# Kernel optimization log

Hardware: AMD Instinct MI355X
Metric: run time of the kernel (lower is better)

The kernel has to match this reference:

```python
import jax, jax.numpy as jnp
import numpy as np

B, T = 65536, 256
E = H = 5

def setup_inputs() -> dict:
    key = jax.random.key(0)
    ks = jax.random.split(key, 8)
    return {
        "x": jax.random.randint(ks[0], (B, T), 0, 2),
        "emb": jax.random.normal(ks[1], (2, E), jnp.float32),
        "W_ih": jax.random.normal(ks[2], (4 * H, E), jnp.float32) * 0.3,
        "W_hh": jax.random.normal(ks[3], (4 * H, H), jnp.float32) * 0.3,
        "b_ih": jax.random.normal(ks[4], (4 * H,), jnp.float32) * 0.1,
        "b_hh": jax.random.normal(ks[5], (4 * H,), jnp.float32) * 0.1,
        "W_lin": jax.random.normal(ks[6], (2, H), jnp.float32) * 0.3,
        "b_lin": jax.random.normal(ks[7], (2,), jnp.float32) * 0.1,
    }

def reference(x, emb, W_ih, W_hh, b_ih, b_hh, W_lin, b_lin):
    # Embedding lookup: [B, T] int -> [B, T, E]
    xe = emb[x]
    # Precompute input contributions to all 4 gates for every timestep: [B, T, 4H]
    gx = jnp.einsum("bte,ge->btg", xe, W_ih) + (b_ih + b_hh)
    Whh_T = W_hh.T  # [H, 4H]

    def step(carry, gx_t):
        h, c = carry  # each [B, H]
        gates = gx_t + h @ Whh_T  # [B, 4H]
        i, f, g, o = jnp.split(gates, 4, axis=-1)  # PyTorch gate order i,f,g,o
        i = jax.nn.sigmoid(i)
        f = jax.nn.sigmoid(f)
        g = jnp.tanh(g)
        o = jax.nn.sigmoid(o)
        c = f * c + i * g
        h = o * jnp.tanh(c)
        return (h, c), None

    h0 = jnp.zeros((x.shape[0], H), xe.dtype)
    c0 = jnp.zeros((x.shape[0], H), xe.dtype)
    # scan over time (axis 1 -> move to leading axis)
    (h_last, _), _ = jax.lax.scan(step, (h0, c0), jnp.swapaxes(gx, 0, 1))
    # Final-step linear head: [B, H] -> [B, 2]
    return h_last @ W_lin.T + b_lin
```

## Files before the change

kernel.cpp:

```cpp
#include <hip/hip_runtime.h>


typedef float v2f __attribute__((ext_vector_type(2)));

constexpr int TT = 256;

__device__ __forceinline__ float fexp2(float v) { return __builtin_amdgcn_exp2f(v); }
__device__ __forceinline__ float frcp(float v)  { return __builtin_amdgcn_rcpf(v); }

__device__ __forceinline__ int pair_row(int p, int h) {
    if (p < 8) return (p >> 1) * 5 + (p & 1) * 2 + h;
    return (p == 8) ? (h ? 9 : 4) : (h ? 19 : 14);
}

__global__ __launch_bounds__(256, 1) void lstm_fused(
    const int* __restrict__ x,
    const float* __restrict__ emb,
    const float* __restrict__ W_ih,
    const float* __restrict__ W_hh,
    const float* __restrict__ b_ih,
    const float* __restrict__ b_hh,
    const float* __restrict__ W_lin,
    const float* __restrict__ b_lin,
    float* __restrict__ out)
{
    const int b = blockIdx.x * blockDim.x + threadIdx.x;

    const float NL2E  = -1.4426950408889634f;
    const float T2L2E =  2.8853900817779268f;
    const v2f ONE = {1.f, 1.f};
    const v2f T2v = {T2L2E, T2L2E};

    v2f bpk[10], dpk[10];
    v2f wpk[5][10];
#pragma unroll
    for (int p = 0; p < 10; ++p) {
        float v0[2], v1[2];
#pragma unroll
        for (int h = 0; h < 2; ++h) {
            const int r = pair_row(p, h);
            const float s = (r >= 10 && r < 15) ? T2L2E : NL2E;
            float g0 = b_ih[r] + b_hh[r], g1 = g0;
#pragma unroll
            for (int e = 0; e < 5; ++e) {
                float w = W_ih[r * 5 + e];
                g0 = fmaf(w, emb[e],     g0);
                g1 = fmaf(w, emb[5 + e], g1);
            }
            v0[h] = s * g0;
            v1[h] = s * (g1 - g0);
#pragma unroll
            for (int k = 0; k < 5; ++k) {
                float w = s * W_hh[r * 5 + k];
                asm volatile("" : "+v"(w));
                wpk[k][p][h] = w;
            }
        }
        asm volatile("" : "+v"(v0[0]), "+v"(v0[1]), "+v"(v1[0]), "+v"(v1[1]));
        bpk[p][0] = v0[0]; bpk[p][1] = v0[1];
        dpk[p][0] = v1[0]; dpk[p][1] = v1[1];
    }

    v2f chat01 = {0.f, 0.f}, chat23 = {0.f, 0.f};
    float chat4 = 0.f;
    v2f h01 = {0.f, 0.f}, h23 = {0.f, 0.f};
    float h4 = 0.f;

    auto step = [&](int xt) {
        const float xtf = (float)xt;
        v2f xv; xv[0] = xtf; xv[1] = xtf;
        v2f g[10];
#pragma unroll
        for (int p = 0; p < 10; ++p)
            g[p] = __builtin_elementwise_fma(xv, dpk[p], bpk[p]);
        const float hk[5] = {h01[0], h01[1], h23[0], h23[1], h4};
#pragma unroll
        for (int k = 0; k < 5; ++k) {
            v2f hv; hv[0] = hk[k]; hv[1] = hk[k];
#pragma unroll
            for (int p = 0; p < 10; ++p)
                g[p] = __builtin_elementwise_fma(wpk[k][p], hv, g[p]);
        }
        v2f E[10];
#pragma unroll
        for (int p = 0; p < 10; ++p) {
            E[p][0] = fexp2(g[p][0]);
            E[p][1] = fexp2(g[p][1]);
        }

        v2f Ai01 = E[0] + ONE, Af01 = E[2] + ONE, Ag01 = E[4] + ONE;
        v2f P01 = Ai01 * Ag01, D01 = P01 * Af01;
        v2f t01 = __builtin_elementwise_fma(T2v, E[4], -T2v);
        v2f N01 = __builtin_elementwise_fma(chat01, P01, t01 * Af01);

        v2f Ai23 = E[1] + ONE, Af23 = E[3] + ONE, Ag23 = E[5] + ONE;
        v2f P23 = Ai23 * Ag23, D23 = P23 * Af23;
        v2f t23 = __builtin_elementwise_fma(T2v, E[5], -T2v);
        v2f N23 = __builtin_elementwise_fma(chat23, P23, t23 * Af23);

        v2f AiAf4 = E[8] + ONE;
        v2f AgAo4 = E[9] + ONE;
        float P4 = AiAf4[0] * AgAo4[0];
        float D4 = P4 * AiAf4[1];
        float t4 = fmaf(T2L2E, E[9][0], -T2L2E);
        float N4 = fmaf(chat4, P4, t4 * AiAf4[1]);

        {
            float R01 = frcp(D01[0] * D01[1]);
            v2f Rv01; Rv01[0] = R01; Rv01[1] = R01;
            chat01 = (N01 * __builtin_shufflevector(D01, D01, 1, 0)) * Rv01;
            float R23 = frcp(D23[0] * D23[1]);
            v2f Rv23; Rv23[0] = R23; Rv23[1] = R23;
            chat23 = (N23 * __builtin_shufflevector(D23, D23, 1, 0)) * Rv23;
            chat4 = N4 * frcp(D4);
        }

        v2f Ec01; Ec01[0] = fexp2(chat01[0]); Ec01[1] = fexp2(chat01[1]);
        v2f Ec23; Ec23[0] = fexp2(chat23[0]); Ec23[1] = fexp2(chat23[1]);
        float Ec4 = fexp2(chat4);

        v2f Dn01 = (E[6] + ONE) * (Ec01 + ONE), Tn01 = Ec01 - ONE;
        v2f Dn23 = (E[7] + ONE) * (Ec23 + ONE), Tn23 = Ec23 - ONE;
        float Dn4 = AgAo4[1] * (Ec4 + 1.f), Tn4 = Ec4 - 1.f;

        {
            float R01 = frcp(Dn01[0] * Dn01[1]);
            v2f Rv01; Rv01[0] = R01; Rv01[1] = R01;
            h01 = (Tn01 * __builtin_shufflevector(Dn01, Dn01, 1, 0)) * Rv01;
            float R23 = frcp(Dn23[0] * Dn23[1]);
            v2f Rv23; Rv23[0] = R23; Rv23[1] = R23;
            h23 = (Tn23 * __builtin_shufflevector(Dn23, Dn23, 1, 0)) * Rv23;
            h4 = Tn4 * frcp(Dn4);
        }
    };

    const int4* xr = reinterpret_cast<const int4*>(x + (size_t)b * TT);
    int4 cur = xr[0];
#pragma unroll 1
    for (int it = 0; it < TT / 4 - 1; ++it) {
        int4 nxt = xr[it + 1];
        step(cur.x); step(cur.y); step(cur.z); step(cur.w);
        cur = nxt;
    }
    step(cur.x); step(cur.y); step(cur.z); step(cur.w);

    const float hfin[5] = {h01[0], h01[1], h23[0], h23[1], h4};
    float o0 = b_lin[0], o1 = b_lin[1];
#pragma unroll
    for (int j = 0; j < 5; ++j) {
        o0 = fmaf(W_lin[j],     hfin[j], o0);
        o1 = fmaf(W_lin[5 + j], hfin[j], o1);
    }
    reinterpret_cast<float2*>(out)[b] = make_float2(o0, o1);
}

extern "C" void kernel_launch(void* const* d_in, const int* in_sizes, int n_in,
                              void* d_out, int out_size, void* d_ws, size_t ws_size,
                              hipStream_t stream) {
    const int* x        = (const int*)d_in[0];
    const float* emb    = (const float*)d_in[1];
    const float* W_ih   = (const float*)d_in[2];
    const float* W_hh   = (const float*)d_in[3];
    const float* b_ih   = (const float*)d_in[4];
    const float* b_hh   = (const float*)d_in[5];
    const float* W_lin  = (const float*)d_in[6];
    const float* b_lin  = (const float*)d_in[7];
    float* out          = (float*)d_out;

    const int B = in_sizes[0] / TT;
    const int block = 256;
    const int grid = B / block;

    lstm_fused<<<grid, block, 0, stream>>>(x, emb, W_ih, W_hh, b_ih, b_hh,
                                           W_lin, b_lin, out);
}
```

Before: 93.72 us.

## Keep recurrent weights in scalar registers and reorder exp/rcp scheduling

Moves four of the five recurrent weight columns into wave-uniform scalar registers via readfirstlane packed as 64-bit values, so the packed FMAs read SGPR operands and VGPR pressure drops. The fifth column stays in vector registers. Output-gate exponentials are deferred past the reciprocal computations so transcendental latency can overlap, and the launch bound is expressed as waves_per_eu(1,1). Risks include SGPR pressure or the compiler copying the weights back into VGPRs, and packed-FMA operand restrictions on scalar sources.

```diff
diff --git a/kernel.cpp b/kernel.cpp
--- a/kernel.cpp
+++ b/kernel.cpp
@@ -13,7 +13,16 @@
     return (p == 8) ? (h ? 9 : 4) : (h ? 19 : 14);
 }
 
-__global__ __launch_bounds__(256, 1) void lstm_fused(
+__device__ __forceinline__ double upack(float w0, float w1) {
+    unsigned lo = (unsigned)__builtin_amdgcn_readfirstlane(__builtin_bit_cast(int, w0));
+    unsigned hi = (unsigned)__builtin_amdgcn_readfirstlane(__builtin_bit_cast(int, w1));
+    unsigned long long u = ((unsigned long long)hi << 32) | lo;
+    return __builtin_bit_cast(double, u);
+}
+
+__global__ __launch_bounds__(256)
+__attribute__((amdgpu_waves_per_eu(1, 1)))
+void lstm_fused(
     const int* __restrict__ x,
     const float* __restrict__ emb,
     const float* __restrict__ W_ih,
@@ -31,11 +40,13 @@
     const v2f ONE = {1.f, 1.f};
     const v2f T2v = {T2L2E, T2L2E};
 
+    double wu[4][10];
+    v2f    wv[10];
     v2f bpk[10], dpk[10];
-    v2f wpk[5][10];
 #pragma unroll
     for (int p = 0; p < 10; ++p) {
-        float v0[2], v1[2];
+        float v0[2], v1[2], w4[2];
+        float wk[4][2];
 #pragma unroll
         for (int h = 0; h < 2; ++h) {
             const int r = pair_row(p, h);
@@ -50,12 +61,13 @@
             v0[h] = s * g0;
             v1[h] = s * (g1 - g0);
 #pragma unroll
-            for (int k = 0; k < 5; ++k) {
-                float w = s * W_hh[r * 5 + k];
-                asm volatile("" : "+v"(w));
-                wpk[k][p][h] = w;
-            }
-        }
+            for (int k = 0; k < 4; ++k) wk[k][h] = s * W_hh[r * 5 + k];
+            w4[h] = s * W_hh[r * 5 + 4];
+        }
+#pragma unroll
+        for (int k = 0; k < 4; ++k) wu[k][p] = upack(wk[k][0], wk[k][1]);
+        asm volatile("" : "+v"(w4[0]), "+v"(w4[1]));
+        wv[p][0] = w4[0]; wv[p][1] = w4[1];
         asm volatile("" : "+v"(v0[0]), "+v"(v0[1]), "+v"(v1[0]), "+v"(v1[1]));
         bpk[p][0] = v0[0]; bpk[p][1] = v0[1];
         dpk[p][0] = v1[0]; dpk[p][1] = v1[1];
@@ -73,63 +85,79 @@
 #pragma unroll
         for (int p = 0; p < 10; ++p)
             g[p] = __builtin_elementwise_fma(xv, dpk[p], bpk[p]);
-        const float hk[5] = {h01[0], h01[1], h23[0], h23[1], h4};
-#pragma unroll
-        for (int k = 0; k < 5; ++k) {
+        const float hk[4] = {h01[0], h01[1], h23[0], h23[1]};
+#pragma unroll
+        for (int k = 0; k < 4; ++k) {
             v2f hv; hv[0] = hk[k]; hv[1] = hk[k];
 #pragma unroll
+            for (int p = 0; p < 10; ++p) {
+                v2f w = __builtin_bit_cast(v2f, wu[k][p]);
+                g[p] = __builtin_elementwise_fma(w, hv, g[p]);
+            }
+        }
+        {
+            v2f hv; hv[0] = h4; hv[1] = h4;
+#pragma unroll
             for (int p = 0; p < 10; ++p)
-                g[p] = __builtin_elementwise_fma(wpk[k][p], hv, g[p]);
-        }
-        v2f E[10];
-#pragma unroll
-        for (int p = 0; p < 10; ++p) {
-            E[p][0] = fexp2(g[p][0]);
-            E[p][1] = fexp2(g[p][1]);
-        }
-
-        v2f Ai01 = E[0] + ONE, Af01 = E[2] + ONE, Ag01 = E[4] + ONE;
+                g[p] = __builtin_elementwise_fma(wv[p], hv, g[p]);
+        }
+
+        v2f E0, E1, E2, E3, E4, E5, E8, E9;
+        E0[0] = fexp2(g[0][0]); E0[1] = fexp2(g[0][1]);
+        E1[0] = fexp2(g[1][0]); E1[1] = fexp2(g[1][1]);
+        E2[0] = fexp2(g[2][0]); E2[1] = fexp2(g[2][1]);
+        E3[0] = fexp2(g[3][0]); E3[1] = fexp2(g[3][1]);
+        E4[0] = fexp2(g[4][0]); E4[1] = fexp2(g[4][1]);
+        E5[0] = fexp2(g[5][0]); E5[1] = fexp2(g[5][1]);
+        E8[0] = fexp2(g[8][0]); E8[1] = fexp2(g[8][1]);
+        E9[0] = fexp2(g[9][0]); E9[1] = fexp2(g[9][1]);
+
+        v2f Ai01 = E0 + ONE, Af01 = E2 + ONE, Ag01 = E4 + ONE;
         v2f P01 = Ai01 * Ag01, D01 = P01 * Af01;
-        v2f t01 = __builtin_elementwise_fma(T2v, E[4], -T2v);
+        v2f t01 = __builtin_elementwise_fma(T2v, E4, -T2v);
         v2f N01 = __builtin_elementwise_fma(chat01, P01, t01 * Af01);
 
-        v2f Ai23 = E[1] + ONE, Af23 = E[3] + ONE, Ag23 = E[5] + ONE;
+        v2f Ai23 = E1 + ONE, Af23 = E3 + ONE, Ag23 = E5 + ONE;
         v2f P23 = Ai23 * Ag23, D23 = P23 * Af23;
-        v2f t23 = __builtin_elementwise_fma(T2v, E[5], -T2v);
+        v2f t23 = __builtin_elementwise_fma(T2v, E5, -T2v);
         v2f N23 = __builtin_elementwise_fma(chat23, P23, t23 * Af23);
 
-        v2f AiAf4 = E[8] + ONE;
-        v2f AgAo4 = E[9] + ONE;
+        v2f AiAf4 = E8 + ONE;
+        v2f AgAo4 = E9 + ONE;
         float P4 = AiAf4[0] * AgAo4[0];
         float D4 = P4 * AiAf4[1];
-        float t4 = fmaf(T2L2E, E[9][0], -T2L2E);
+        float t4 = fmaf(T2L2E, E9[0], -T2L2E);
         float N4 = fmaf(chat4, P4, t4 * AiAf4[1]);
 
+        float R01 = frcp(D01[0] * D01[1]);
+        float R23 = frcp(D23[0] * D23[1]);
+        float R4g = frcp(D4);
+        v2f E6, E7;
+        E6[0] = fexp2(g[6][0]); E6[1] = fexp2(g[6][1]);
+        E7[0] = fexp2(g[7][0]); E7[1] = fexp2(g[7][1]);
         {
-            float R01 = frcp(D01[0] * D01[1]);
             v2f Rv01; Rv01[0] = R01; Rv01[1] = R01;
             chat01 = (N01 * __builtin_shufflevector(D01, D01, 1, 0)) * Rv01;
-            float R23 = frcp(D23[0] * D23[1]);
             v2f Rv23; Rv23[0] = R23; Rv23[1] = R23;
             chat23 = (N23 * __builtin_shufflevector(D23, D23, 1, 0)) * Rv23;
-            chat4 = N4 * frcp(D4);
+            chat4 = N4 * R4g;
         }
 
         v2f Ec01; Ec01[0] = fexp2(chat01[0]); Ec01[1] = fexp2(chat01[1]);
         v2f Ec23; Ec23[0] = fexp2(chat23[0]); Ec23[1] = fexp2(chat23[1]);
         float Ec4 = fexp2(chat4);
 
-        v2f Dn01 = (E[6] + ONE) * (Ec01 + ONE), Tn01 = Ec01 - ONE;
-        v2f Dn23 = (E[7] + ONE) * (Ec23 + ONE), Tn23 = Ec23 - ONE;
+        v2f Dn01 = (E6 + ONE) * (Ec01 + ONE), Tn01 = Ec01 - ONE;
+        v2f Dn23 = (E7 + ONE) * (Ec23 + ONE), Tn23 = Ec23 - ONE;
         float Dn4 = AgAo4[1] * (Ec4 + 1.f), Tn4 = Ec4 - 1.f;
 
         {
-            float R01 = frcp(Dn01[0] * Dn01[1]);
-            v2f Rv01; Rv01[0] = R01; Rv01[1] = R01;
-            h01 = (Tn01 * __builtin_shufflevector(Dn01, Dn01, 1, 0)) * Rv01;
-            float R23 = frcp(Dn23[0] * Dn23[1]);
-            v2f Rv23; Rv23[0] = R23; Rv23[1] = R23;
-            h23 = (Tn23 * __builtin_shufflevector(Dn23, Dn23, 1, 0)) * Rv23;
+            float S01 = frcp(Dn01[0] * Dn01[1]);
+            v2f Sv01; Sv01[0] = S01; Sv01[1] = S01;
+            h01 = (Tn01 * __builtin_shufflevector(Dn01, Dn01, 1, 0)) * Sv01;
+            float S23 = frcp(Dn23[0] * Dn23[1]);
+            v2f Sv23; Sv23[0] = S23; Sv23[1] = S23;
+            h23 = (Tn23 * __builtin_shufflevector(Dn23, Dn23, 1, 0)) * Sv23;
             h4 = Tn4 * frcp(Dn4);
         }
     };
```

After: 93.17 us. No clear change (-0.6%).
